# Optimization experiments

Measured on AMD Instinct MI355X. Metric: run time of the kernel, lower is better.

## Reference

```python
import jax, jax.numpy as jnp
import numpy as np

HIDDEN = 512
INPUT = 512
BATCH = 16384


def _quant_dequant(w):
    # mirrors torch: scale = max(|w|)/127 + 1e-8; int8 round-clamp; dequantize
    scale = jnp.max(jnp.abs(w)) / 127.0 + 1e-8
    q = jnp.clip(jnp.round(w / scale), -128, 127)
    return q * scale


def setup_inputs() -> dict:
    key = jax.random.key(0)
    ks = jax.random.split(key, 7)
    x = jax.random.normal(ks[0], (BATCH, INPUT), dtype=jnp.float32)
    h_prev = jax.random.normal(ks[1], (BATCH, HIDDEN), dtype=jnp.float32)
    c_prev = jax.random.normal(ks[2], (BATCH, HIDDEN), dtype=jnp.float32)
    w_ih = _quant_dequant(jax.random.normal(ks[3], (4 * HIDDEN, INPUT), dtype=jnp.float32) * 0.05)
    w_hh = _quant_dequant(jax.random.normal(ks[4], (4 * HIDDEN, HIDDEN), dtype=jnp.float32) * 0.05)
    bias_ih = jax.random.normal(ks[5], (4 * HIDDEN,), dtype=jnp.float32) * 0.05
    bias_hh = jax.random.normal(ks[6], (4 * HIDDEN,), dtype=jnp.float32) * 0.05
    return {"x": x, "h_prev": h_prev, "c_prev": c_prev,
            "w_ih": w_ih, "w_hh": w_hh, "bias_ih": bias_ih, "bias_hh": bias_hh}


def reference(x, h_prev, c_prev, w_ih, w_hh, bias_ih, bias_hh):
    # gates: [B, 4H]
    gates = x @ w_ih.T + bias_ih + h_prev @ w_hh.T + bias_hh
    i_g, f_g, g_g, o_g = jnp.split(gates, 4, axis=1)
    i_g = jax.nn.sigmoid(i_g)
    f_g = jax.nn.sigmoid(f_g)
    g_g = jnp.tanh(g_g)
    o_g = jax.nn.sigmoid(o_g)
    c_new = f_g * c_prev + i_g * g_g
    h_new = o_g * jnp.tanh(c_new)
    return (h_new, c_new)
```

## Files before the change

kernel.cpp:

```cpp
#include <hip/hip_runtime.h>


typedef __attribute__((ext_vector_type(4))) int int4v;
typedef __attribute__((ext_vector_type(8))) short short8;
typedef __attribute__((ext_vector_type(4))) float f32x4;
typedef unsigned int u32;
typedef unsigned short u16;
typedef unsigned char u8;

#define BATCH 16384
#define HID 512
#define KTOT 1024
#define BM 256
#define KSTEPS 16
#define TILEA_BYTES 16384
#define TILEW_BYTES 8192
#define BUFBYTES 24576
#define NBM 64
#define NBN 16
#define WSA_BYTES ((size_t)NBM * KSTEPS * TILEA_BYTES)
#define WSW_BYTES ((size_t)NBN * KSTEPS * TILEW_BYTES)
#define SCALE_OFF (WSA_BYTES + WSW_BYTES)
#define PART_OFF (SCALE_OFF + 65536)
#define SW_OFF (PART_OFF + 2048)
#define WS_NEEDED (SW_OFF + 64)
#define PACKA_BLOCKS (BATCH / 4)

__device__ __forceinline__ float sigmoidf_(float v) { return 1.0f / (1.0f + __expf(-v)); }
__device__ __forceinline__ float tanhf_(float v) { return 1.0f - 2.0f / (__expf(2.0f * v) + 1.0f); }

__device__ __forceinline__ void gload_lds16(const void* g, void* l) {
    __builtin_amdgcn_global_load_lds(
        (const __attribute__((address_space(1))) u32*)g,
        (__attribute__((address_space(3))) u32*)l, 16, 0, 0);
}

__device__ __forceinline__ u32 pack4(float a, float b, float c, float d, float inv) {
    int q0 = (int)rintf(a * inv), q1 = (int)rintf(b * inv);
    int q2 = (int)rintf(c * inv), q3 = (int)rintf(d * inv);
    return (q0 & 255) | ((q1 & 255) << 8) | ((q2 & 255) << 16) | ((q3 & 255) << 24);
}

__device__ __forceinline__ u32 swz_pos(u32 row, u32 c) {
    return ((row >> 1) << 3) | ((((row & 1) << 2) | c) ^ ((row >> 1) & 7));
}

__global__ __launch_bounds__(256) void pack_a_wmax(
    const float* __restrict__ x, const float* __restrict__ h_prev,
    const float* __restrict__ w_ih, const float* __restrict__ w_hh,
    u8* __restrict__ wsA, float* __restrict__ aScale, float* __restrict__ part)
{
    const u32 t = threadIdx.x;
    if (blockIdx.x >= PACKA_BLOCKS) {
        const u32 b = blockIdx.x - PACKA_BLOCKS;
        const float* src = (b < 256) ? (w_ih + (size_t)b * 4096)
                                     : (w_hh + (size_t)(b - 256) * 4096);
        float am = 0.f;
        const float4* p = (const float4*)src + t;
        #pragma unroll
        for (int j = 0; j < 4; ++j) {
            float4 v = p[j * 256];
            am = fmaxf(am, fmaxf(fmaxf(fabsf(v.x), fabsf(v.y)), fmaxf(fabsf(v.z), fabsf(v.w))));
        }
        #pragma unroll
        for (int o = 32; o >= 1; o >>= 1) am = fmaxf(am, __shfl_xor(am, o, 64));
        __shared__ float red[4];
        if ((t & 63) == 0) red[t >> 6] = am;
        __syncthreads();
        if (t == 0) part[b] = fmaxf(fmaxf(red[0], red[1]), fmaxf(red[2], red[3]));
        return;
    }
    __shared__ float4 stg[4][256];
    const u32 lane = t & 63;
    const u32 wv = t >> 6;
    const u32 m = blockIdx.x * 4 + wv;
    const float4* xr = (const float4*)(x + (size_t)m * 512);
    const float4* hr = (const float4*)(h_prev + (size_t)m * 512);
    float4 v[4];
    v[0] = xr[lane];
    v[1] = xr[lane + 64];
    v[2] = hr[lane];
    v[3] = hr[lane + 64];
    float am = 0.f;
    #pragma unroll
    for (int j = 0; j < 4; ++j)
        am = fmaxf(am, fmaxf(fmaxf(fabsf(v[j].x), fabsf(v[j].y)),
                             fmaxf(fabsf(v[j].z), fabsf(v[j].w))));
    #pragma unroll
    for (int o = 32; o >= 1; o >>= 1) am = fmaxf(am, __shfl_xor(am, o, 64));
    const float inv = (am > 0.f) ? 127.0f / am : 0.f;
    if (lane == 0) aScale[m] = am * (1.0f / 127.0f);

    #pragma unroll
    for (int j = 0; j < 4; ++j)
        stg[wv][j * 64 + (lane ^ ((lane >> 2) & 7))] = v[j];
    u32 wds[4];
    #pragma unroll
    for (int s = 0; s < 4; ++s) {
        float4 w = stg[wv][(4 * lane + s) ^ (lane & 7)];
        wds[s] = pack4(w.x, w.y, w.z, w.w, inv);
    }
    const u32 bm = m >> 8, row = m & 255;
    const u32 ks = lane >> 2, clog = lane & 3;
    const u32 pos = swz_pos(row, clog);
    int4v val = {(int)wds[0], (int)wds[1], (int)wds[2], (int)wds[3]};
    *(int4v*)(wsA + ((((size_t)bm * KSTEPS + ks) << 10) + pos) * 16) = val;
}

__global__ __launch_bounds__(256) void pack_w(
    const float* __restrict__ w_ih, const float* __restrict__ w_hh,
    const float* __restrict__ part, u8* __restrict__ wsW, float* __restrict__ swOut)
{
    const u32 t = threadIdx.x;
    float am = fmaxf(part[t], part[t + 256]);
    #pragma unroll
    for (int o = 32; o >= 1; o >>= 1) am = fmaxf(am, __shfl_xor(am, o, 64));
    __shared__ float red[4];
    if ((t & 63) == 0) red[t >> 6] = am;
    __syncthreads();
    const float wmax = fmaxf(fmaxf(red[0], red[1]), fmaxf(red[2], red[3]));
    const float inv = 127.0f / wmax;
    if (blockIdx.x == 0 && t == 0) *swOut = wmax * (1.0f / 127.0f);

    const u32 widx = blockIdx.x * 256 + t;
    const u32 tile = widx >> 9;
    const u32 p = widx & 511;
    const u32 wrowHalf = p >> 3;
    const u32 slot = (p & 7) ^ (wrowHalf & 7);
    const u32 wrow = (wrowHalf << 1) | (slot >> 2);
    const u32 clog = slot & 3;
    const u32 ks = tile & 15, bn = tile >> 4;
    const u32 g = wrow >> 5, rr = wrow & 31;
    const u32 wr = g * 512 + bn * 32 + rr;
    const u32 kglob = ks * 64 + clog * 16;
    const float* src = (kglob < 512) ? (w_ih + (size_t)wr * 512 + kglob)
                                     : (w_hh + (size_t)wr * 512 + (kglob - 512));
    u32 wds[4];
    #pragma unroll
    for (int j = 0; j < 4; ++j) {
        float4 v = *((const float4*)src + j);
        wds[j] = pack4(v.x, v.y, v.z, v.w, inv);
    }
    int4v val = {(int)wds[0], (int)wds[1], (int)wds[2], (int)wds[3]};
    *(int4v*)(wsW + (size_t)widx * 16) = val;
}

__global__ __launch_bounds__(256, 2) void lstm_gemm(
    const u8* __restrict__ wsA, const u8* __restrict__ wsW,
    const float* __restrict__ aScale, const float* __restrict__ swPtr,
    const float* __restrict__ c_prev,
    const float* __restrict__ b_ih, const float* __restrict__ b_hh,
    float* __restrict__ h_out, float* __restrict__ c_out)
{
    __shared__ u8 sB0[BUFBYTES];
    __shared__ u8 sB1[BUFBYTES];

    const int t = threadIdx.x;
    const u32 bid = blockIdx.x;
    const u32 xcd = bid & 7;
    const u32 slot = bid >> 3;
    const int bm = (int)((slot >> 4) * 8 + xcd);
    const int bn = (int)(slot & 15);
    const int n0 = bn * 32;
    const int rowBase = bm * BM;

    const int lane = t & 63;
    const int wv = t >> 6;
    const int colin = lane & 15;
    const int quad = lane >> 4;
    const int stageOff = t * 16;

    int4v acc[4][2][4];
    #pragma unroll
    for (int rf = 0; rf < 4; ++rf)
        #pragma unroll
        for (int cc = 0; cc < 2; ++cc)
            #pragma unroll
            for (int g = 0; g < 4; ++g)
                acc[rf][cc][g] = (int4v){0, 0, 0, 0};

    const char* gA = (const char*)wsA + (size_t)bm * KSTEPS * TILEA_BYTES;
    const char* gW = (const char*)wsW + (size_t)bn * KSTEPS * TILEW_BYTES;

    u32 aoffs[4], woffs[8];
    #pragma unroll
    for (int rf = 0; rf < 4; ++rf) {
        const u32 row = (u32)(wv * 64 + rf * 16 + colin);
        aoffs[rf] = swz_pos(row, (u32)quad) * 16;
    }
    #pragma unroll
    for (int cc = 0; cc < 2; ++cc)
        #pragma unroll
        for (int g = 0; g < 4; ++g) {
            const u32 wrow = (u32)(g * 32 + cc * 16 + colin);
            woffs[cc * 4 + g] = 16384u + swz_pos(wrow, (u32)quad) * 16;
        }

#define STAGE(KS, DST)                                                          \
    {                                                                           \
        _Pragma("unroll")                                                       \
        for (int j = 0; j < 4; ++j)                                             \
            gload_lds16(gA + (size_t)(KS) * TILEA_BYTES + j * 4096 + stageOff,  \
                        (char*)(DST) + j * 4096 + stageOff);                    \
        _Pragma("unroll")                                                       \
        for (int j = 0; j < 2; ++j)                                             \
            gload_lds16(gW + (size_t)(KS) * TILEW_BYTES + j * 4096 + stageOff,  \
                        (char*)(DST) + 16384 + j * 4096 + stageOff);            \
    }

#define COMPUTE(SRC)                                                            \
    {                                                                           \
        int4v af[4];                                                            \
        _Pragma("unroll")                                                       \
        for (int rf = 0; rf < 4; ++rf)                                          \
            af[rf] = *(const int4v*)((const char*)(SRC) + aoffs[rf]);           \
        int4v bfr[2][4];                                                        \
        _Pragma("unroll")                                                       \
        for (int cc = 0; cc < 2; ++cc)                                          \
            _Pragma("unroll")                                                   \
            for (int g = 0; g < 4; ++g)                                         \
                bfr[cc][g] = *(const int4v*)((const char*)(SRC) + woffs[cc * 4 + g]); \
        _Pragma("unroll")                                                       \
        for (int rf = 0; rf < 4; ++rf)                                          \
            _Pragma("unroll")                                                   \
            for (int cc = 0; cc < 2; ++cc)                                      \
                _Pragma("unroll")                                               \
                for (int g = 0; g < 4; ++g)                                     \
                    acc[rf][cc][g] = __builtin_amdgcn_mfma_i32_16x16x64_i8(     \
                        af[rf], bfr[cc][g], acc[rf][cc][g], 0, 0, 0);           \
    }

    STAGE(0, sB0);
    __syncthreads();
    #pragma unroll 1
    for (int ks = 0; ks < KSTEPS; ks += 2) {
        STAGE(ks + 1, sB1);
        COMPUTE(sB0);
        __syncthreads();
        if (ks + 2 < KSTEPS) STAGE(ks + 2, sB0);
        COMPUTE(sB1);
        __syncthreads();
    }
#undef STAGE
#undef COMPUTE

    const float sw = *swPtr;
    float rsc[4][4];
    #pragma unroll
    for (int rf = 0; rf < 4; ++rf)
        #pragma unroll
        for (int reg = 0; reg < 4; ++reg)
            rsc[rf][reg] = aScale[rowBase + wv * 64 + rf * 16 + quad * 4 + reg] * sw;

    float bsum[2][4];
    #pragma unroll
    for (int cc = 0; cc < 2; ++cc) {
        const int colg = n0 + cc * 16 + colin;
        #pragma unroll
        for (int g = 0; g < 4; ++g)
            bsum[cc][g] = b_ih[g * 512 + colg] + b_hh[g * 512 + colg];
    }

    #pragma unroll
    for (int rf = 0; rf < 4; ++rf)
        #pragma unroll
        for (int cc = 0; cc < 2; ++cc) {
            const int colg = n0 + cc * 16 + colin;
            #pragma unroll
            for (int reg = 0; reg < 4; ++reg) {
                const int row = rowBase + wv * 64 + rf * 16 + quad * 4 + reg;
                const size_t off = (size_t)row * 512 + colg;
                const float s = rsc[rf][reg];
                const float ig = (float)acc[rf][cc][0][reg] * s + bsum[cc][0];
                const float fg = (float)acc[rf][cc][1][reg] * s + bsum[cc][1];
                const float gg = (float)acc[rf][cc][2][reg] * s + bsum[cc][2];
                const float og = (float)acc[rf][cc][3][reg] * s + bsum[cc][3];
                const float cp = __builtin_nontemporal_load(c_prev + off);
                const float cn = sigmoidf_(fg) * cp + sigmoidf_(ig) * tanhf_(gg);
                const float hn = sigmoidf_(og) * tanhf_(cn);
                __builtin_nontemporal_store(hn, h_out + off);
                __builtin_nontemporal_store(cn, c_out + off);
            }
        }
}

#define LDSK 72
__device__ __forceinline__ u16 f2bf(float f) {
    u32 u = __builtin_bit_cast(u32, f);
    u += 0x7FFFu + ((u >> 16) & 1u);
    return (u16)(u >> 16);
}
__global__ __launch_bounds__(256, 3) void lstm_fused_v1(
    const float* __restrict__ x, const float* __restrict__ h_prev,
    const float* __restrict__ c_prev, const float* __restrict__ w_ih,
    const float* __restrict__ w_hh, const float* __restrict__ b_ih,
    const float* __restrict__ b_hh, float* __restrict__ h_out,
    float* __restrict__ c_out)
{
    __shared__ u16 sA[128][LDSK];
    __shared__ u16 sW[128][LDSK];
    const int t = threadIdx.x;
    const int bn = blockIdx.x & 15, bm = blockIdx.x >> 4;
    const int n0 = bn * 32, rowBase = bm * 128;
    const int srow = t >> 4, scol = t & 15;
    const int lane = t & 63, wv = t >> 6, colin = lane & 15, quad = lane >> 4;
    f32x4 acc[2][2][4];
    #pragma unroll
    for (int rf = 0; rf < 2; ++rf)
        #pragma unroll
        for (int cc = 0; cc < 2; ++cc)
            #pragma unroll
            for (int g = 0; g < 4; ++g) acc[rf][cc][g] = (f32x4){0.f, 0.f, 0.f, 0.f};
    for (int k0 = 0; k0 < KTOT; k0 += 64) {
        const int kk = (k0 < 512) ? k0 : (k0 - 512);
        const float* aSrc = (k0 < 512) ? x : h_prev;
        const float* wSrc = (k0 < 512) ? w_ih : w_hh;
        __syncthreads();
        #pragma unroll
        for (int p = 0; p < 8; ++p) {
            const int r = srow + p * 16;
            const float4 av = *(const float4*)(aSrc + (size_t)(rowBase + r) * 512 + kk + scol * 4);
            ushort4 ap; ap.x = f2bf(av.x); ap.y = f2bf(av.y); ap.z = f2bf(av.z); ap.w = f2bf(av.w);
            *(ushort4*)&sA[r][scol * 4] = ap;
            const int gate = r >> 5, rr = r & 31;
            const float4 wvv = *(const float4*)(wSrc + (size_t)(gate * 512 + n0 + rr) * 512 + kk + scol * 4);
            ushort4 wp; wp.x = f2bf(wvv.x); wp.y = f2bf(wvv.y); wp.z = f2bf(wvv.z); wp.w = f2bf(wvv.w);
            *(ushort4*)&sW[r][scol * 4] = wp;
        }
        __syncthreads();
        #pragma unroll
        for (int ks = 0; ks < 2; ++ks) {
            short8 af[2];
            #pragma unroll
            for (int rf = 0; rf < 2; ++rf)
                af[rf] = *(const short8*)&sA[wv * 32 + rf * 16 + colin][ks * 32 + quad * 8];
            short8 bfr[2][4];
            #pragma unroll
            for (int cc = 0; cc < 2; ++cc)
                #pragma unroll
                for (int g = 0; g < 4; ++g)
                    bfr[cc][g] = *(const short8*)&sW[g * 32 + cc * 16 + colin][ks * 32 + quad * 8];
            #pragma unroll
            for (int rf = 0; rf < 2; ++rf)
                #pragma unroll
                for (int cc = 0; cc < 2; ++cc)
                    #pragma unroll
                    for (int g = 0; g < 4; ++g)
                        acc[rf][cc][g] = __builtin_amdgcn_mfma_f32_16x16x32_bf16(
                            af[rf], bfr[cc][g], acc[rf][cc][g], 0, 0, 0);
        }
    }
    float bsum[2][4];
    #pragma unroll
    for (int cc = 0; cc < 2; ++cc) {
        const int colg = n0 + cc * 16 + colin;
        #pragma unroll
        for (int g = 0; g < 4; ++g) bsum[cc][g] = b_ih[g * 512 + colg] + b_hh[g * 512 + colg];
    }
    #pragma unroll
    for (int rf = 0; rf < 2; ++rf)
        #pragma unroll
        for (int cc = 0; cc < 2; ++cc) {
            const int colg = n0 + cc * 16 + colin;
            #pragma unroll
            for (int reg = 0; reg < 4; ++reg) {
                const int row = rowBase + wv * 32 + rf * 16 + quad * 4 + reg;
                const size_t off = (size_t)row * 512 + colg;
                const float ig = acc[rf][cc][0][reg] + bsum[cc][0];
                const float fg = acc[rf][cc][1][reg] + bsum[cc][1];
                const float gg = acc[rf][cc][2][reg] + bsum[cc][2];
                const float og = acc[rf][cc][3][reg] + bsum[cc][3];
                const float cp = c_prev[off];
                const float cn = sigmoidf_(fg) * cp + sigmoidf_(ig) * tanhf_(gg);
                const float hn = sigmoidf_(og) * tanhf_(cn);
                h_out[off] = hn;
                c_out[off] = cn;
            }
        }
}

extern "C" void kernel_launch(void* const* d_in, const int* in_sizes, int n_in,
                              void* d_out, int out_size, void* d_ws, size_t ws_size,
                              hipStream_t stream) {
    const float* x      = (const float*)d_in[0];
    const float* h_prev = (const float*)d_in[1];
    const float* c_prev = (const float*)d_in[2];
    const float* w_ih   = (const float*)d_in[3];
    const float* w_hh   = (const float*)d_in[4];
    const float* b_ih   = (const float*)d_in[5];
    const float* b_hh   = (const float*)d_in[6];
    float* h_out = (float*)d_out;
    float* c_out = h_out + (size_t)BATCH * HID;

    if (ws_size >= WS_NEEDED) {
        u8* wsA = (u8*)d_ws;
        u8* wsW = (u8*)d_ws + WSA_BYTES;
        float* aScale = (float*)((char*)d_ws + SCALE_OFF);
        float* part   = (float*)((char*)d_ws + PART_OFF);
        float* swOut  = (float*)((char*)d_ws + SW_OFF);
        pack_a_wmax<<<PACKA_BLOCKS + 512, 256, 0, stream>>>(x, h_prev, w_ih, w_hh,
                                                            wsA, aScale, part);
        pack_w<<<512, 256, 0, stream>>>(w_ih, w_hh, part, wsW, swOut);
        lstm_gemm<<<NBM * NBN, 256, 0, stream>>>(wsA, wsW, aScale, swOut, c_prev,
                                                 b_ih, b_hh, h_out, c_out);
    } else {
        lstm_fused_v1<<<128 * 16, 256, 0, stream>>>(x, h_prev, c_prev, w_ih, w_hh,
                                                    b_ih, b_hh, h_out, c_out);
    }
}
```

Before: 210.5 us.

## Single-buffer LDS staging and raise occupancy target to four blocks per CU

Replaces the double-buffered LDS pipeline with one 24KB buffer that is loaded and then consumed each k-step, with barriers before and after the load. Launch bounds are raised from 2 to 4 blocks per CU so more waves can hide global-load latency, trading in-block prefetch overlap for inter-block overlap. The higher occupancy target constrains registers for the 128 int32 accumulators and may cause spills, and each step now waits on its own load.

```diff
diff --git a/kernel.cpp b/kernel.cpp
--- a/kernel.cpp
+++ b/kernel.cpp
@@ -145,15 +145,14 @@
     *(int4v*)(wsW + (size_t)widx * 16) = val;
 }
 
-__global__ __launch_bounds__(256, 2) void lstm_gemm(
+__global__ __launch_bounds__(256, 4) void lstm_gemm(
     const u8* __restrict__ wsA, const u8* __restrict__ wsW,
     const float* __restrict__ aScale, const float* __restrict__ swPtr,
     const float* __restrict__ c_prev,
     const float* __restrict__ b_ih, const float* __restrict__ b_hh,
     float* __restrict__ h_out, float* __restrict__ c_out)
 {
-    __shared__ u8 sB0[BUFBYTES];
-    __shared__ u8 sB1[BUFBYTES];
+    __shared__ u8 sB[BUFBYTES];
 
     const int t = threadIdx.x;
     const u32 bid = blockIdx.x;
@@ -196,53 +195,38 @@
             woffs[cc * 4 + g] = 16384u + swz_pos(wrow, (u32)quad) * 16;
         }
 
-#define STAGE(KS, DST)                                                          \
-    {                                                                           \
-        _Pragma("unroll")                                                       \
-        for (int j = 0; j < 4; ++j)                                             \
-            gload_lds16(gA + (size_t)(KS) * TILEA_BYTES + j * 4096 + stageOff,  \
-                        (char*)(DST) + j * 4096 + stageOff);                    \
-        _Pragma("unroll")                                                       \
-        for (int j = 0; j < 2; ++j)                                             \
-            gload_lds16(gW + (size_t)(KS) * TILEW_BYTES + j * 4096 + stageOff,  \
-                        (char*)(DST) + 16384 + j * 4096 + stageOff);            \
-    }
-
-#define COMPUTE(SRC)                                                            \
-    {                                                                           \
-        int4v af[4];                                                            \
-        _Pragma("unroll")                                                       \
-        for (int rf = 0; rf < 4; ++rf)                                          \
-            af[rf] = *(const int4v*)((const char*)(SRC) + aoffs[rf]);           \
-        int4v bfr[2][4];                                                        \
-        _Pragma("unroll")                                                       \
-        for (int cc = 0; cc < 2; ++cc)                                          \
-            _Pragma("unroll")                                                   \
-            for (int g = 0; g < 4; ++g)                                         \
-                bfr[cc][g] = *(const int4v*)((const char*)(SRC) + woffs[cc * 4 + g]); \
-        _Pragma("unroll")                                                       \
-        for (int rf = 0; rf < 4; ++rf)                                          \
-            _Pragma("unroll")                                                   \
-            for (int cc = 0; cc < 2; ++cc)                                      \
-                _Pragma("unroll")                                               \
-                for (int g = 0; g < 4; ++g)                                     \
-                    acc[rf][cc][g] = __builtin_amdgcn_mfma_i32_16x16x64_i8(     \
-                        af[rf], bfr[cc][g], acc[rf][cc][g], 0, 0, 0);           \
-    }
-
-    STAGE(0, sB0);
-    __syncthreads();
     #pragma unroll 1
-    for (int ks = 0; ks < KSTEPS; ks += 2) {
-        STAGE(ks + 1, sB1);
-        COMPUTE(sB0);
-        __syncthreads();
-        if (ks + 2 < KSTEPS) STAGE(ks + 2, sB0);
-        COMPUTE(sB1);
-        __syncthreads();
-    }
-#undef STAGE
-#undef COMPUTE
+    for (int ks = 0; ks < KSTEPS; ++ks) {
+        __syncthreads();
+        #pragma unroll
+        for (int j = 0; j < 4; ++j)
+            gload_lds16(gA + (size_t)ks * TILEA_BYTES + j * 4096 + stageOff,
+                        (char*)sB + j * 4096 + stageOff);
+        #pragma unroll
+        for (int j = 0; j < 2; ++j)
+            gload_lds16(gW + (size_t)ks * TILEW_BYTES + j * 4096 + stageOff,
+                        (char*)sB + 16384 + j * 4096 + stageOff);
+        __syncthreads();
+
+        int4v af[4];
+        #pragma unroll
+        for (int rf = 0; rf < 4; ++rf)
+            af[rf] = *(const int4v*)((const char*)sB + aoffs[rf]);
+        int4v bfr[2][4];
+        #pragma unroll
+        for (int cc = 0; cc < 2; ++cc)
+            #pragma unroll
+            for (int g = 0; g < 4; ++g)
+                bfr[cc][g] = *(const int4v*)((const char*)sB + woffs[cc * 4 + g]);
+        #pragma unroll
+        for (int rf = 0; rf < 4; ++rf)
+            #pragma unroll
+            for (int cc = 0; cc < 2; ++cc)
+                #pragma unroll
+                for (int g = 0; g < 4; ++g)
+                    acc[rf][cc][g] = __builtin_amdgcn_mfma_i32_16x16x64_i8(
+                        af[rf], bfr[cc][g], acc[rf][cc][g], 0, 0, 0);
+    }
 
     const float sw = *swPtr;
     float rsc[4][4];
```

New measurement: 434.6 us. +106.5%, slower.
